# Optimization experiments

Measured on AMD Instinct MI355X. Metric: run time of the kernel, lower is better.

## Reference

```python
import jax, jax.numpy as jnp
import numpy as np

N, F_IN, H, W = 8192, 512, 256, 64
THRESHOLD = 0.8


def setup_inputs() -> dict:
    key = jax.random.key(0)
    ks = jax.random.split(key, 9)
    def lin(k, fan_in, shape):
        return (jax.random.normal(k, shape, jnp.float32) / np.sqrt(fan_in)).astype(jnp.float32)
    return {
        "state_batch": jax.random.normal(ks[0], (N, F_IN), jnp.float32),
        "W1": lin(ks[1], F_IN, (F_IN, H)), "b1": jnp.zeros((H,), jnp.float32),
        "W2": lin(ks[2], H, (H, H)),      "b2": jnp.zeros((H,), jnp.float32),
        "Wq": lin(ks[3], H, (H, W)),      "bq": jnp.zeros((W,), jnp.float32),
        "Wh": lin(ks[4], W, (W, 1)),      "bh": jnp.zeros((1,), jnp.float32),
    }


def reference(state_batch, W1, b1, W2, b2, Wq, bq, Wh, bh):
    # classical encoder: two ReLU Linear layers
    enc = jax.nn.relu(state_batch @ W1 + b1)
    enc = jax.nn.relu(enc @ W2 + b2)
    # quantum layer surrogate: bounded features in [-1, 1] like PauliZ expectations
    q_out = jnp.tanh(enc @ Wq + bq)                      # [N, W]

    # pairwise squared-cosine fidelity (vectorized Gram matrix, replaces
    # the itertools.combinations + .item() host-sync loop)
    qn = q_out / (jnp.linalg.norm(q_out, axis=1, keepdims=True) + 1e-12)
    fid = (qn @ qn.T) ** 2                               # [N, N]

    n = q_out.shape[0]
    # graph edges: fid >= threshold, no self loops; edge weight = 1.0
    mask = (fid >= THRESHOLD) & (~jnp.eye(n, dtype=bool))
    deg = mask.sum(axis=1)
    wsum = mask.astype(q_out.dtype).sum(axis=1)          # all weights are 1.0
    # mean neighbor weight; nodes with no neighbors keep their own feature (factor 1)
    mean_w = jnp.where(deg > 0, wsum / jnp.maximum(deg, 1).astype(q_out.dtype), 1.0)
    attn = q_out * mean_w[:, None]                       # [N, W]

    agg = attn.sum(axis=0, keepdims=True)                # [1, W]
    out = (agg @ Wh + bh).squeeze(-1)                    # [1]
    return out
```

## Files before the change

### kernel.cpp

```cpp
#include <hip/hip_runtime.h>
#include <hip/hip_bf16.h>
#include <math.h>


#define N_ROWS 8192
#define F_IN   512
#define H_DIM  256
#define W_DIM  64

#define LDS_S 520
#define LDE   264

#define W1_FRAGS (16 * 16 * 64)
#define W2_FRAGS (16 * 8 * 64)
#define WQ_FRAGS (4 * 8 * 64)
#define PREP_T   (W1_FRAGS + W2_FRAGS + WQ_FRAGS)
#define PREP_BLOCKS ((PREP_T + 255) / 256)

using bf16x8 = __attribute__((ext_vector_type(8))) short;
using bf16x4 = __attribute__((ext_vector_type(4))) short;
using f32x4  = __attribute__((ext_vector_type(4))) float;
typedef __hip_bfloat16 bf16;

__device__ __forceinline__ void split2(float v, bf16& hi, bf16& lo) {
    bf16 h = __float2bfloat16(v);
    hi = h;
    lo = __float2bfloat16(v - __bfloat162float(h));
}

__global__ __launch_bounds__(256) void prep_w(
    const float* __restrict__ W1, const float* __restrict__ W2,
    const float* __restrict__ Wq, const float* __restrict__ bh,
    bf16* __restrict__ W1h, bf16* __restrict__ W1l,
    bf16* __restrict__ W2h, bf16* __restrict__ W2l,
    bf16* __restrict__ Wqh, bf16* __restrict__ Wql,
    float* __restrict__ out)
{
    if (blockIdx.x == 0 && threadIdx.x == 0) out[0] = bh[0];
    int gid = blockIdx.x * 256 + threadIdx.x;
    if (gid < W1_FRAGS) {
        const int l = gid & 63, ks = (gid >> 6) & 15, n16 = gid >> 10;
        const int n = n16 * 16 + (l & 15);
        const int kb = ks * 32 + ((l >> 4) << 3);
        bf16 hb[8], lb[8];
        #pragma unroll
        for (int j = 0; j < 8; ++j)
            split2(W1[(size_t)(kb + j) * H_DIM + n], hb[j], lb[j]);
        *(bf16x8*)(W1h + (size_t)gid * 8) = *(const bf16x8*)hb;
        *(bf16x8*)(W1l + (size_t)gid * 8) = *(const bf16x8*)lb;
        return;
    }
    gid -= W1_FRAGS;
    if (gid < W2_FRAGS) {
        const int l = gid & 63, ks = (gid >> 6) & 7, n16 = gid >> 9;
        const int n = n16 * 16 + (l & 15);
        const int kb = ks * 32 + ((l >> 4) << 3);
        bf16 hb[8], lb[8];
        #pragma unroll
        for (int j = 0; j < 8; ++j)
            split2(W2[(size_t)(kb + j) * H_DIM + n], hb[j], lb[j]);
        *(bf16x8*)(W2h + (size_t)gid * 8) = *(const bf16x8*)hb;
        *(bf16x8*)(W2l + (size_t)gid * 8) = *(const bf16x8*)lb;
        return;
    }
    gid -= W2_FRAGS;
    if (gid < WQ_FRAGS) {
        const int l = gid & 63, ks = (gid >> 6) & 7, n16 = gid >> 9;
        const int n = n16 * 16 + (l & 15);
        const int kb = ks * 32 + ((l >> 4) << 3);
        bf16 hb[8], lb[8];
        #pragma unroll
        for (int j = 0; j < 8; ++j)
            split2(Wq[(size_t)(kb + j) * W_DIM + n], hb[j], lb[j]);
        *(bf16x8*)(Wqh + (size_t)gid * 8) = *(const bf16x8*)hb;
        *(bf16x8*)(Wql + (size_t)gid * 8) = *(const bf16x8*)lb;
    }
}

__global__ __launch_bounds__(512) void fused_chain(
    const float* __restrict__ S,
    const bf16* __restrict__ W1h, const bf16* __restrict__ W1l,
    const bf16* __restrict__ W2h, const bf16* __restrict__ W2l,
    const bf16* __restrict__ Wqh, const bf16* __restrict__ Wql,
    const float* __restrict__ b1, const float* __restrict__ b2,
    const float* __restrict__ bq, const float* __restrict__ Wh,
    float* __restrict__ out)
{
    __shared__ bf16 Ssh[32 * LDS_S];
    __shared__ bf16 Ssl[32 * LDS_S];
    __shared__ bf16 E1h[32 * LDE];
    __shared__ bf16 E1l[32 * LDE];
    __shared__ bf16 E2h[32 * LDE];
    __shared__ bf16 E2l[32 * LDE];
    __shared__ float red[2][64];

    const int t = threadIdx.x;
    const int lane = t & 63;
    const int w = t >> 6, quad = lane >> 4, m16 = t & 15;
    const int row0 = blockIdx.x * 32;

    #pragma unroll
    for (int i = 0; i < 8; ++i) {
        const int idx = i * 2048 + t * 4;
        const int r = idx >> 9, c = idx & 511;
        float4 sv = *(const float4*)(S + (size_t)(row0 + r) * F_IN + c);
        bf16 hb[4], lb[4];
        split2(sv.x, hb[0], lb[0]); split2(sv.y, hb[1], lb[1]);
        split2(sv.z, hb[2], lb[2]); split2(sv.w, hb[3], lb[3]);
        *(bf16x4*)&Ssh[r * LDS_S + c] = *(const bf16x4*)hb;
        *(bf16x4*)&Ssl[r * LDS_S + c] = *(const bf16x4*)lb;
    }
    __syncthreads();

    f32x4 acc[2][2] = {};
    #pragma unroll
    for (int ks = 0; ks < F_IN / 32; ++ks) {
        const int ao = ks * 32 + quad * 8;
        bf16x8 a0h = *(const bf16x8*)&Ssh[m16 * LDS_S + ao];
        bf16x8 a0l = *(const bf16x8*)&Ssl[m16 * LDS_S + ao];
        bf16x8 a1h = *(const bf16x8*)&Ssh[(16 + m16) * LDS_S + ao];
        bf16x8 a1l = *(const bf16x8*)&Ssl[(16 + m16) * LDS_S + ao];
        #pragma unroll
        for (int jj = 0; jj < 2; ++jj) {
            const size_t off = ((size_t)(((2 * w + jj) * 16 + ks) * 64 + lane)) * 8;
            bf16x8 b_h = *(const bf16x8*)(W1h + off);
            bf16x8 b_l = *(const bf16x8*)(W1l + off);
            acc[0][jj] = __builtin_amdgcn_mfma_f32_16x16x32_bf16(a0h, b_h, acc[0][jj], 0, 0, 0);
            acc[0][jj] = __builtin_amdgcn_mfma_f32_16x16x32_bf16(a0l, b_h, acc[0][jj], 0, 0, 0);
            acc[0][jj] = __builtin_amdgcn_mfma_f32_16x16x32_bf16(a0h, b_l, acc[0][jj], 0, 0, 0);
            acc[1][jj] = __builtin_amdgcn_mfma_f32_16x16x32_bf16(a1h, b_h, acc[1][jj], 0, 0, 0);
            acc[1][jj] = __builtin_amdgcn_mfma_f32_16x16x32_bf16(a1l, b_h, acc[1][jj], 0, 0, 0);
            acc[1][jj] = __builtin_amdgcn_mfma_f32_16x16x32_bf16(a1h, b_l, acc[1][jj], 0, 0, 0);
        }
    }
    #pragma unroll
    for (int i = 0; i < 2; ++i)
        #pragma unroll
        for (int jj = 0; jj < 2; ++jj) {
            const int c = 32 * w + jj * 16 + m16;
            const float bv = b1[c];
            #pragma unroll
            for (int r = 0; r < 4; ++r) {
                const int rr = i * 16 + quad * 4 + r;
                float vv = fmaxf(acc[i][jj][r] + bv, 0.0f);
                split2(vv, E1h[rr * LDE + c], E1l[rr * LDE + c]);
            }
        }
    __syncthreads();

    #pragma unroll
    for (int i = 0; i < 2; ++i)
        #pragma unroll
        for (int jj = 0; jj < 2; ++jj)
            acc[i][jj] = (f32x4){0.f, 0.f, 0.f, 0.f};
    #pragma unroll
    for (int ks = 0; ks < H_DIM / 32; ++ks) {
        const int ao = ks * 32 + quad * 8;
        bf16x8 a0h = *(const bf16x8*)&E1h[m16 * LDE + ao];
        bf16x8 a0l = *(const bf16x8*)&E1l[m16 * LDE + ao];
        bf16x8 a1h = *(const bf16x8*)&E1h[(16 + m16) * LDE + ao];
        bf16x8 a1l = *(const bf16x8*)&E1l[(16 + m16) * LDE + ao];
        #pragma unroll
        for (int jj = 0; jj < 2; ++jj) {
            const size_t off = ((size_t)(((2 * w + jj) * 8 + ks) * 64 + lane)) * 8;
            bf16x8 b_h = *(const bf16x8*)(W2h + off);
            bf16x8 b_l = *(const bf16x8*)(W2l + off);
            acc[0][jj] = __builtin_amdgcn_mfma_f32_16x16x32_bf16(a0h, b_h, acc[0][jj], 0, 0, 0);
            acc[0][jj] = __builtin_amdgcn_mfma_f32_16x16x32_bf16(a0l, b_h, acc[0][jj], 0, 0, 0);
            acc[0][jj] = __builtin_amdgcn_mfma_f32_16x16x32_bf16(a0h, b_l, acc[0][jj], 0, 0, 0);
            acc[1][jj] = __builtin_amdgcn_mfma_f32_16x16x32_bf16(a1h, b_h, acc[1][jj], 0, 0, 0);
            acc[1][jj] = __builtin_amdgcn_mfma_f32_16x16x32_bf16(a1l, b_h, acc[1][jj], 0, 0, 0);
            acc[1][jj] = __builtin_amdgcn_mfma_f32_16x16x32_bf16(a1h, b_l, acc[1][jj], 0, 0, 0);
        }
    }
    #pragma unroll
    for (int i = 0; i < 2; ++i)
        #pragma unroll
        for (int jj = 0; jj < 2; ++jj) {
            const int c = 32 * w + jj * 16 + m16;
            const float bv = b2[c];
            #pragma unroll
            for (int r = 0; r < 4; ++r) {
                const int rr = i * 16 + quad * 4 + r;
                float vv = fmaxf(acc[i][jj][r] + bv, 0.0f);
                split2(vv, E2h[rr * LDE + c], E2l[rr * LDE + c]);
            }
        }
    __syncthreads();

    {
        const int rf = w >> 2, cf = w & 3;
        f32x4 acc3 = {0.f, 0.f, 0.f, 0.f};
        #pragma unroll
        for (int ks = 0; ks < H_DIM / 32; ++ks) {
            const int ao = ks * 32 + quad * 8;
            bf16x8 a_h = *(const bf16x8*)&E2h[(rf * 16 + m16) * LDE + ao];
            bf16x8 a_l = *(const bf16x8*)&E2l[(rf * 16 + m16) * LDE + ao];
            const size_t off = ((size_t)((cf * 8 + ks) * 64 + lane)) * 8;
            bf16x8 b_h = *(const bf16x8*)(Wqh + off);
            bf16x8 b_l = *(const bf16x8*)(Wql + off);
            acc3 = __builtin_amdgcn_mfma_f32_16x16x32_bf16(a_h, b_h, acc3, 0, 0, 0);
            acc3 = __builtin_amdgcn_mfma_f32_16x16x32_bf16(a_l, b_h, acc3, 0, 0, 0);
            acc3 = __builtin_amdgcn_mfma_f32_16x16x32_bf16(a_h, b_l, acc3, 0, 0, 0);
        }
        const int c = cf * 16 + m16;
        const float bv = bq[c];
        float v = 0.f;
        #pragma unroll
        for (int r = 0; r < 4; ++r)
            v += tanhf(acc3[r] + bv);
        v += __shfl_xor(v, 16, 64);
        v += __shfl_xor(v, 32, 64);
        if (quad == 0) red[rf][c] = v;
        __syncthreads();
        if (t < W_DIM) {
            float s = (red[0][t] + red[1][t]) * Wh[t];
            #pragma unroll
            for (int o = 32; o > 0; o >>= 1) s += __shfl_down(s, o);
            if (t == 0) atomicAdd(out, s);
        }
    }
}

extern "C" void kernel_launch(void* const* d_in, const int* in_sizes, int n_in,
                              void* d_out, int out_size, void* d_ws, size_t ws_size,
                              hipStream_t stream) {
    const float* state = (const float*)d_in[0];
    const float* W1    = (const float*)d_in[1];
    const float* b1    = (const float*)d_in[2];
    const float* W2    = (const float*)d_in[3];
    const float* b2    = (const float*)d_in[4];
    const float* Wq    = (const float*)d_in[5];
    const float* bq    = (const float*)d_in[6];
    const float* Wh    = (const float*)d_in[7];
    const float* bh    = (const float*)d_in[8];

    bf16* p = (bf16*)d_ws;
    bf16* W1h = p; p += (size_t)H_DIM * F_IN;
    bf16* W1l = p; p += (size_t)H_DIM * F_IN;
    bf16* W2h = p; p += (size_t)H_DIM * H_DIM;
    bf16* W2l = p; p += (size_t)H_DIM * H_DIM;
    bf16* Wqh = p; p += (size_t)W_DIM * H_DIM;
    bf16* Wql = p; p += (size_t)W_DIM * H_DIM;

    prep_w<<<PREP_BLOCKS, 256, 0, stream>>>(
        W1, W2, Wq, bh, W1h, W1l, W2h, W2l, Wqh, Wql, (float*)d_out);

    fused_chain<<<N_ROWS / 32, 512, 0, stream>>>(
        state, W1h, W1l, W2h, W2l, Wqh, Wql, b1, b2, bq, Wh, (float*)d_out);
}
```

Before: 97.37 us.

## Fuse weight prep into main kernel using cooperative grid sync

Merges the weight split-to-bf16 prep kernel into the fused chain kernel and launches it cooperatively, with each block converting a slice of the weight fragments before a grid-wide barrier. This removes one kernel launch and overlaps weight conversion with the per-block state-tile staging. The cost is a grid-wide sync across 256 blocks of 512 threads, and the launch depends on all blocks being co-resident, which cooperative launch requires (large LDS use per block).

Result: slower. 142.9 us (+46.7%).

```diff
diff --git a/kernel.cpp b/kernel.cpp
--- a/kernel.cpp
+++ b/kernel.cpp
@@ -1,6 +1,9 @@
 #include <hip/hip_runtime.h>
+#include <hip/hip_cooperative_groups.h>
 #include <hip/hip_bf16.h>
 #include <math.h>
+
+namespace cg = cooperative_groups;
 
 
 #define N_ROWS 8192
@@ -15,7 +18,7 @@
 #define W2_FRAGS (16 * 8 * 64)
 #define WQ_FRAGS (4 * 8 * 64)
 #define PREP_T   (W1_FRAGS + W2_FRAGS + WQ_FRAGS)
-#define PREP_BLOCKS ((PREP_T + 255) / 256)
+#define PREP_PER_BLK ((PREP_T + 255) / 256)
 
 using bf16x8 = __attribute__((ext_vector_type(8))) short;
 using bf16x4 = __attribute__((ext_vector_type(4))) short;
@@ -28,62 +31,16 @@
     lo = __float2bfloat16(v - __bfloat162float(h));
 }
 
-__global__ __launch_bounds__(256) void prep_w(
+__global__ __launch_bounds__(512) void fused_all(
+    const float* __restrict__ S,
     const float* __restrict__ W1, const float* __restrict__ W2,
-    const float* __restrict__ Wq, const float* __restrict__ bh,
+    const float* __restrict__ Wq,
+    const float* __restrict__ b1, const float* __restrict__ b2,
+    const float* __restrict__ bq, const float* __restrict__ Wh,
+    const float* __restrict__ bh,
     bf16* __restrict__ W1h, bf16* __restrict__ W1l,
     bf16* __restrict__ W2h, bf16* __restrict__ W2l,
     bf16* __restrict__ Wqh, bf16* __restrict__ Wql,
-    float* __restrict__ out)
-{
-    if (blockIdx.x == 0 && threadIdx.x == 0) out[0] = bh[0];
-    int gid = blockIdx.x * 256 + threadIdx.x;
-    if (gid < W1_FRAGS) {
-        const int l = gid & 63, ks = (gid >> 6) & 15, n16 = gid >> 10;
-        const int n = n16 * 16 + (l & 15);
-        const int kb = ks * 32 + ((l >> 4) << 3);
-        bf16 hb[8], lb[8];
-        #pragma unroll
-        for (int j = 0; j < 8; ++j)
-            split2(W1[(size_t)(kb + j) * H_DIM + n], hb[j], lb[j]);
-        *(bf16x8*)(W1h + (size_t)gid * 8) = *(const bf16x8*)hb;
-        *(bf16x8*)(W1l + (size_t)gid * 8) = *(const bf16x8*)lb;
-        return;
-    }
-    gid -= W1_FRAGS;
-    if (gid < W2_FRAGS) {
-        const int l = gid & 63, ks = (gid >> 6) & 7, n16 = gid >> 9;
-        const int n = n16 * 16 + (l & 15);
-        const int kb = ks * 32 + ((l >> 4) << 3);
-        bf16 hb[8], lb[8];
-        #pragma unroll
-        for (int j = 0; j < 8; ++j)
-            split2(W2[(size_t)(kb + j) * H_DIM + n], hb[j], lb[j]);
-        *(bf16x8*)(W2h + (size_t)gid * 8) = *(const bf16x8*)hb;
-        *(bf16x8*)(W2l + (size_t)gid * 8) = *(const bf16x8*)lb;
-        return;
-    }
-    gid -= W2_FRAGS;
-    if (gid < WQ_FRAGS) {
-        const int l = gid & 63, ks = (gid >> 6) & 7, n16 = gid >> 9;
-        const int n = n16 * 16 + (l & 15);
-        const int kb = ks * 32 + ((l >> 4) << 3);
-        bf16 hb[8], lb[8];
-        #pragma unroll
-        for (int j = 0; j < 8; ++j)
-            split2(Wq[(size_t)(kb + j) * W_DIM + n], hb[j], lb[j]);
-        *(bf16x8*)(Wqh + (size_t)gid * 8) = *(const bf16x8*)hb;
-        *(bf16x8*)(Wql + (size_t)gid * 8) = *(const bf16x8*)lb;
-    }
-}
-
-__global__ __launch_bounds__(512) void fused_chain(
-    const float* __restrict__ S,
-    const bf16* __restrict__ W1h, const bf16* __restrict__ W1l,
-    const bf16* __restrict__ W2h, const bf16* __restrict__ W2l,
-    const bf16* __restrict__ Wqh, const bf16* __restrict__ Wql,
-    const float* __restrict__ b1, const float* __restrict__ b2,
-    const float* __restrict__ bq, const float* __restrict__ Wh,
     float* __restrict__ out)
 {
     __shared__ bf16 Ssh[32 * LDS_S];
@@ -99,6 +56,45 @@
     const int w = t >> 6, quad = lane >> 4, m16 = t & 15;
     const int row0 = blockIdx.x * 32;
 
+    if (blockIdx.x == 0 && t == 0) out[0] = bh[0];
+
+    if (t < PREP_PER_BLK) {
+        int item = blockIdx.x * PREP_PER_BLK + t;
+        if (item < W1_FRAGS) {
+            const int l = item & 63, ks = (item >> 6) & 15, n16 = item >> 10;
+            const int n = n16 * 16 + (l & 15);
+            const int kb = ks * 32 + ((l >> 4) << 3);
+            bf16 hb[8], lb[8];
+            #pragma unroll
+            for (int j = 0; j < 8; ++j)
+                split2(W1[(size_t)(kb + j) * H_DIM + n], hb[j], lb[j]);
+            *(bf16x8*)(W1h + (size_t)item * 8) = *(const bf16x8*)hb;
+            *(bf16x8*)(W1l + (size_t)item * 8) = *(const bf16x8*)lb;
+        } else if (item < W1_FRAGS + W2_FRAGS) {
+            const int it = item - W1_FRAGS;
+            const int l = it & 63, ks = (it >> 6) & 7, n16 = it >> 9;
+            const int n = n16 * 16 + (l & 15);
+            const int kb = ks * 32 + ((l >> 4) << 3);
+            bf16 hb[8], lb[8];
+            #pragma unroll
+            for (int j = 0; j < 8; ++j)
+                split2(W2[(size_t)(kb + j) * H_DIM + n], hb[j], lb[j]);
+            *(bf16x8*)(W2h + (size_t)it * 8) = *(const bf16x8*)hb;
+            *(bf16x8*)(W2l + (size_t)it * 8) = *(const bf16x8*)lb;
+        } else if (item < PREP_T) {
+            const int it = item - W1_FRAGS - W2_FRAGS;
+            const int l = it & 63, ks = (it >> 6) & 7, n16 = it >> 9;
+            const int n = n16 * 16 + (l & 15);
+            const int kb = ks * 32 + ((l >> 4) << 3);
+            bf16 hb[8], lb[8];
+            #pragma unroll
+            for (int j = 0; j < 8; ++j)
+                split2(Wq[(size_t)(kb + j) * W_DIM + n], hb[j], lb[j]);
+            *(bf16x8*)(Wqh + (size_t)it * 8) = *(const bf16x8*)hb;
+            *(bf16x8*)(Wql + (size_t)it * 8) = *(const bf16x8*)lb;
+        }
+    }
+
     #pragma unroll
     for (int i = 0; i < 8; ++i) {
         const int idx = i * 2048 + t * 4;
@@ -110,7 +106,8 @@
         *(bf16x4*)&Ssh[r * LDS_S + c] = *(const bf16x4*)hb;
         *(bf16x4*)&Ssl[r * LDS_S + c] = *(const bf16x4*)lb;
     }
-    __syncthreads();
+
+    cg::this_grid().sync();
 
     f32x4 acc[2][2] = {};
     #pragma unroll
@@ -242,10 +239,14 @@
     bf16* W2l = p; p += (size_t)H_DIM * H_DIM;
     bf16* Wqh = p; p += (size_t)W_DIM * H_DIM;
     bf16* Wql = p; p += (size_t)W_DIM * H_DIM;
-
-    prep_w<<<PREP_BLOCKS, 256, 0, stream>>>(
-        W1, W2, Wq, bh, W1h, W1l, W2h, W2l, Wqh, Wql, (float*)d_out);
-
-    fused_chain<<<N_ROWS / 32, 512, 0, stream>>>(
-        state, W1h, W1l, W2h, W2l, Wqh, Wql, b1, b2, bq, Wh, (float*)d_out);
+    float* outp = (float*)d_out;
+
+    void* args[] = {
+        (void*)&state, (void*)&W1, (void*)&W2, (void*)&Wq,
+        (void*)&b1, (void*)&b2, (void*)&bq, (void*)&Wh, (void*)&bh,
+        (void*)&W1h, (void*)&W1l, (void*)&W2h, (void*)&W2l,
+        (void*)&Wqh, (void*)&Wql, (void*)&outp};
+
+    hipLaunchCooperativeKernel((void*)fused_all, dim3(N_ROWS / 32), dim3(512),
+                               args, 0, stream);
 }
```
